# Kernel tuning notes

Measured on AMD Instinct MI355X. Metric: run time of the kernel, lower is better.

The kernel has to match this reference:

```python
import jax, jax.numpy as jnp
import numpy as np

ALPHA = 0.2  # LeakyReLU negative slope
NEG_INF = -1.0e12


def setup_inputs() -> dict:
    key = jax.random.key(0)
    ks = jax.random.split(key, 8)
    N, F, D, H, M, Q = 4096, 512, 64, 4, 2, 128
    x = jax.random.normal(ks[0], (N, F), dtype=jnp.float32)
    adj = jax.random.randint(ks[1], (M, N, N), 0, 2, dtype=jnp.int32)
    W = jax.random.normal(ks[2], (H, F, D), dtype=jnp.float32) * 0.07
    a1 = jax.random.normal(ks[3], (H, D), dtype=jnp.float32) * 0.15
    a2 = jax.random.normal(ks[4], (H, D), dtype=jnp.float32) * 0.15
    Ws = jax.random.normal(ks[5], (H * D, Q), dtype=jnp.float32) * 0.1
    bs = jax.random.normal(ks[6], (1, Q), dtype=jnp.float32) * 0.1
    q_sem = jax.random.normal(ks[7], (Q, 1), dtype=jnp.float32) * 0.15
    return {"x": x, "adj": adj, "W": W, "a1": a1, "a2": a2,
            "Ws": Ws, "bs": bs, "q_sem": q_sem}


def reference(x, adj, W, a1, a2, Ws, bs, q_sem):
    N = x.shape[0]
    # Wh is identical across meta-paths (dropout disabled / eval mode)
    Wh = jnp.einsum('nf,hfd->hnd', x, W)            # [H,N,D]
    s1 = jnp.einsum('hnd,hd->hn', Wh, a1)           # Wh @ a[:D]
    s2 = jnp.einsum('hnd,hd->hn', Wh, a2)           # Wh @ a[D:]

    def metapath(adj_m):
        # e[h,i,j] = leaky_relu(s1[h,i] + s2[h,j]); mask by adjacency
        e = jax.nn.leaky_relu(s1[:, :, None] + s2[:, None, :], negative_slope=ALPHA)
        e = jnp.where(adj_m[None, :, :] > 0, e, NEG_INF)
        att = jax.nn.softmax(e, axis=2)             # softmax over neighbors (dim=1 in torch [N,N])
        h = jax.nn.elu(jnp.einsum('hnm,hmd->hnd', att, Wh))
        return jnp.transpose(h, (1, 0, 2)).reshape(N, -1)  # concat heads -> [N, H*D]

    Z = jax.vmap(metapath)(adj)                     # [M, N, H*D]
    z = jnp.transpose(Z, (1, 0, 2))                 # [N, M, H*D]

    # Semantic attention (faithful to original, incl. softmax over dim=1 of [M,1])
    Whs = jnp.tanh(jnp.einsum('nmf,fq->nmq', z, Ws) + bs)   # [N,M,Q]
    w = jnp.einsum('nmq,qo->nmo', Whs, q_sem).mean(0)        # [M,1]
    beta = jax.nn.softmax(w, axis=1)                          # [M,1]
    return (beta[None, :, :] * z).sum(axis=1)                 # [N, H*D]
```

## Files before the change

kernel.cpp:

```cpp
#include <hip/hip_runtime.h>
#include <hip/hip_fp16.h>
#include <stdint.h>

#define NN 4096
#define FF 512
#define DD 64
#define HH 4
#define MM 2
#define LOG2E 1.44269504088896340736f
#define ALPHA_LR 0.2f

typedef float f32x4 __attribute__((ext_vector_type(4)));
typedef _Float16 f16x8 __attribute__((ext_vector_type(8)));
typedef _Float16 f16x2 __attribute__((ext_vector_type(2)));

union H4 { ushort4 u; _Float16 h[4]; };
union V8 { f16x8 v; f16x2 p[4]; };

__device__ inline float fast_exp2(float x) { return __builtin_amdgcn_exp2f(x); }
__device__ inline float fast_rcp(float x) { return __builtin_amdgcn_rcpf(x); }
__device__ inline f32x4 mfma16(f16x8 a, f16x8 b, f32x4 c) {
    return __builtin_amdgcn_mfma_f32_16x16x32_f16(a, b, c, 0, 0, 0);
}
__device__ inline f16x2 pkrtz(float a, float b) {
    return __builtin_bit_cast(f16x2, __builtin_amdgcn_cvt_pkrtz(a, b));
}
__device__ inline uint32_t enc_f32(float f) {
    uint32_t u = __float_as_uint(f);
    return (u & 0x80000000u) ? ~u : (u | 0x80000000u);
}
__device__ inline float dec_f32(uint32_t k) {
    uint32_t u = (k & 0x80000000u) ? (k ^ 0x80000000u) : ~k;
    return __uint_as_float(u);
}

__global__ __launch_bounds__(256) void k_conv_x(const float* __restrict__ x,
                                                _Float16* __restrict__ xh,
                                                uint32_t* __restrict__ m4a) {
    int t = blockIdx.x * 256 + threadIdx.x;
    if (t < HH) m4a[t] = 0u;
    float4 v = ((const float4*)x)[t];
    H4 o;
    o.h[0] = (_Float16)v.x; o.h[1] = (_Float16)v.y;
    o.h[2] = (_Float16)v.z; o.h[3] = (_Float16)v.w;
    ((ushort4*)xh)[t] = o.u;
}

__global__ __launch_bounds__(256) void k_conv_w(const float* __restrict__ W,
                                                _Float16* __restrict__ wt) {
    int t = blockIdx.x * 256 + threadIdx.x;
    int c = t >> 9, f = t & 511;
    int h = c >> 6, d = c & 63;
    wt[t] = (_Float16)W[(h * FF + f) * DD + d];
}

__global__ __launch_bounds__(256) void k_pack(const int* __restrict__ adj,
                                              unsigned long long* __restrict__ bitsT) {
    const long long total = (long long)MM * NN * NN;
    const long long stride = 2048LL * 256;
    long long tid = (long long)blockIdx.x * 256 + threadIdx.x;
    for (long long e = tid; e < total; e += stride) {
        unsigned long long msk = __ballot(adj[e] != 0);
        if ((threadIdx.x & 63) == 0) {
            long long q = e >> 6;
            int m  = (int)(q >> 18);
            int rem = (int)(q & 262143);
            int i  = rem >> 6;
            int jw = rem & 63;
            bitsT[((size_t)m * 64 + jw) * NN + i] = msk;
        }
    }
}

__global__ __launch_bounds__(512) void k_wh(const _Float16* __restrict__ xh,
                                            const _Float16* __restrict__ wt,
                                            _Float16* __restrict__ whT) {
    const int wave = threadIdx.x >> 6;
    const int h    = wave & 3;
    const int th   = wave >> 2;
    const int lane = threadIdx.x & 63;
    const int iL   = lane & 15;
    const int quad = lane >> 4;
    const int i0   = blockIdx.x * 16;

    f32x4 acc[2];
    acc[0] = (f32x4){0.f, 0.f, 0.f, 0.f};
    acc[1] = (f32x4){0.f, 0.f, 0.f, 0.f};

    const _Float16* arow  = xh + (size_t)(i0 + iL) * FF + quad * 8;
    const _Float16* bbase = wt + (size_t)(h * 64 + th * 32 + iL) * FF + quad * 8;

    for (int kc = 0; kc < FF; kc += 32) {
        f16x8 a = *(const f16x8*)(arow + kc);
        #pragma unroll
        for (int u = 0; u < 2; ++u) {
            f16x8 b = *(const f16x8*)(bbase + (size_t)(16 * u) * FF + kc);
            acc[u] = mfma16(a, b, acc[u]);
        }
    }
    #pragma unroll
    for (int u = 0; u < 2; ++u) {
        H4 o;
        #pragma unroll
        for (int r = 0; r < 4; ++r) o.h[r] = (_Float16)acc[u][r];
        *(ushort4*)(whT + (size_t)(h * 64 + th * 32 + 16 * u + iL) * NN + i0 + quad * 4) = o.u;
    }
}

__global__ __launch_bounds__(64) void k_s(const _Float16* __restrict__ whT,
                                          const float* __restrict__ a1,
                                          const float* __restrict__ a2,
                                          float* __restrict__ s1L,
                                          float* __restrict__ s2L,
                                          uint32_t* __restrict__ m4a) {
    int b = blockIdx.x;
    int h = b >> 6;
    int n = (b & 63) * 64 + threadIdx.x;
    float s1 = 0.f, s2 = 0.f;
    #pragma unroll 8
    for (int d = 0; d < DD; ++d) {
        float w = (float)whT[(size_t)(h * 64 + d) * NN + n];
        s1 += w * a1[h * 64 + d];
        s2 += w * a2[h * 64 + d];
    }
    float s2l = s2 * LOG2E;
    s1L[h * NN + n] = s1 * LOG2E;
    s2L[h * NN + n] = s2l;
    float mx = s2l;
    #pragma unroll
    for (int off = 32; off > 0; off >>= 1) mx = fmaxf(mx, __shfl_down(mx, off));
    if (threadIdx.x == 0) atomicMax(m4a + h, enc_f32(mx));
}

__global__ __launch_bounds__(512, 2) void k_attn(const _Float16* __restrict__ whT,
                                                 const float* __restrict__ s1L,
                                                 const float* __restrict__ s2L,
                                                 const uint32_t* __restrict__ m4a,
                                                 const unsigned long long* __restrict__ bitsT,
                                                 float* __restrict__ out) {
    __shared__ __align__(16) float xr[4][MM][4][16][16];
    __shared__ __align__(16) float dr[4][MM][16];

    const int tid  = threadIdx.x;
    const int wave = tid >> 6;
    const int lane = tid & 63;
    const int iL   = lane & 15;
    const int quad = lane >> 4;
    const int h    = blockIdx.x & 3;
    const int i0   = (blockIdx.x >> 2) * 64;

    const float m4 = dec_f32(m4a[h]);
    float A[4], B[4];
    #pragma unroll
    for (int s = 0; s < 4; ++s) {
        float s1i = s1L[h * NN + i0 + 16 * s + iL];
        float vv  = s1i + m4;
        float cii = fmaxf(vv, ALPHA_LR * vv);
        A[s] = s1i - cii;
        B[s] = ALPHA_LR * s1i - cii;
    }

    f32x4 acc[4][MM][4];
    f32x4 accD[4][MM];
    #pragma unroll
    for (int s = 0; s < 4; ++s)
        #pragma unroll
        for (int m = 0; m < MM; ++m) {
            accD[s][m] = (f32x4){0.f, 0.f, 0.f, 0.f};
            #pragma unroll
            for (int t = 0; t < 4; ++t) acc[s][m][t] = (f32x4){0.f, 0.f, 0.f, 0.f};
        }

    f16x8 bones;
    #pragma unroll
    for (int e = 0; e < 8; ++e) bones[e] = (_Float16)1.0f;

    const float* s2row = s2L + h * NN;
    const _Float16* brow = whT + (size_t)(h * 64 + iL) * NN;
    const int qshift = quad * 8;
    const int jbase = wave * 512;

    const unsigned long long* pB[MM][4];
    #pragma unroll
    for (int m = 0; m < MM; ++m)
        #pragma unroll
        for (int s = 0; s < 4; ++s)
            pB[m][s] = bitsT + (size_t)m * 64 * NN + i0 + 16 * s + iL;

    for (int it = 0; it < 8; ++it) {
        const int jc = jbase + it * 64;
        const int jw = jc >> 6;
        unsigned long long bm[MM][4];
        #pragma unroll
        for (int m = 0; m < MM; ++m)
            #pragma unroll
            for (int s = 0; s < 4; ++s)
                bm[m][s] = pB[m][s][(size_t)jw * NN];

        #pragma unroll
        for (int half = 0; half < 2; ++half) {
            const int jb = jc + 32 * half;
            f16x8 bfr[4];
            #pragma unroll
            for (int t = 0; t < 4; ++t)
                bfr[t] = *(const f16x8*)(brow + (size_t)(16 * t) * NN + jb + qshift);

            const float* s2p = s2row + jb + qshift;
            float4 sa = *(const float4*)s2p;
            float4 sb = *(const float4*)(s2p + 4);
            float s2v[8] = {sa.x, sa.y, sa.z, sa.w, sb.x, sb.y, sb.z, sb.w};
            const int shft = 32 * half + qshift;

            #pragma unroll
            for (int s = 0; s < 4; ++s) {
                float p[8];
                #pragma unroll
                for (int e = 0; e < 8; ++e) {
                    float arg = fmaxf(s2v[e] + A[s], __builtin_fmaf(ALPHA_LR, s2v[e], B[s]));
                    p[e] = fast_exp2(arg);
                }
                uint32_t rs0 = (uint32_t)(bm[0][s] >> shft);
                uint32_t rs1 = (uint32_t)(bm[1][s] >> shft);
                V8 a0, a1v;
                #pragma unroll
                for (int e = 0; e < 4; ++e) {
                    float q0 = (rs0 & (1u << (2 * e)))     ? p[2 * e]     : 0.f;
                    float q1 = (rs0 & (1u << (2 * e + 1))) ? p[2 * e + 1] : 0.f;
                    float r0 = (rs1 & (1u << (2 * e)))     ? p[2 * e]     : 0.f;
                    float r1 = (rs1 & (1u << (2 * e + 1))) ? p[2 * e + 1] : 0.f;
                    a0.p[e]  = pkrtz(q0, q1);
                    a1v.p[e] = pkrtz(r0, r1);
                }
                #pragma unroll
                for (int t = 0; t < 4; ++t) {
                    acc[s][0][t] = mfma16(a0.v, bfr[t], acc[s][0][t]);
                    acc[s][1][t] = mfma16(a1v.v, bfr[t], acc[s][1][t]);
                }
                accD[s][0] = mfma16(a0.v, bones, accD[s][0]);
                accD[s][1] = mfma16(a1v.v, bones, accD[s][1]);
            }
        }
    }

    #define STORE_SLOT(sl, s)                                                 \
        { _Pragma("unroll") for (int m = 0; m < MM; ++m) {                    \
              _Pragma("unroll") for (int t = 0; t < 4; ++t)                   \
                  *(f32x4*)&xr[sl][m][t][iL][quad * 4] = acc[s][m][t];        \
              if (iL == 0) *(f32x4*)&dr[sl][m][quad * 4] = accD[s][m]; } }
    #define ADD_SLOT(sl, s)                                                   \
        { _Pragma("unroll") for (int m = 0; m < MM; ++m) {                    \
              _Pragma("unroll") for (int t = 0; t < 4; ++t)                   \
                  acc[s][m][t] += *(const f32x4*)&xr[sl][m][t][iL][quad * 4]; \
              accD[s][m] += *(const f32x4*)&dr[sl][m][quad * 4]; } }

    for (int s = 0; s < 4; ++s) {
        __syncthreads();
        if (wave >= 4) STORE_SLOT(wave - 4, s);
        __syncthreads();
        if (wave < 4) ADD_SLOT(wave, s);
        __syncthreads();
        if (wave >= 2 && wave < 4) STORE_SLOT(wave - 2, s);
        __syncthreads();
        if (wave < 2) ADD_SLOT(wave, s);
        __syncthreads();
        if (wave == 1) STORE_SLOT(0, s);
        __syncthreads();
        if (wave == 0) {
            ADD_SLOT(0, s);
            const int i0s = i0 + 16 * s;
            #pragma unroll
            for (int t = 0; t < 4; ++t) {
                #pragma unroll
                for (int r = 0; r < 4; ++r) {
                    float v0 = acc[s][0][t][r] * fast_rcp(accD[s][0][r]);
                    float v1 = acc[s][1][t][r] * fast_rcp(accD[s][1][r]);
                    float e0 = v0 > 0.f ? v0 : (fast_exp2(v0 * LOG2E) - 1.f);
                    float e1 = v1 > 0.f ? v1 : (fast_exp2(v1 * LOG2E) - 1.f);
                    out[(size_t)(i0s + quad * 4 + r) * (HH * DD) + h * 64 + 16 * t + iL] = e0 + e1;
                }
            }
        }
    }
    #undef STORE_SLOT
    #undef ADD_SLOT
}

extern "C" void kernel_launch(void* const* d_in, const int* in_sizes, int n_in,
                              void* d_out, int out_size, void* d_ws, size_t ws_size,
                              hipStream_t stream) {
    const float* x   = (const float*)d_in[0];
    const int*   adj = (const int*)d_in[1];
    const float* W   = (const float*)d_in[2];
    const float* a1  = (const float*)d_in[3];
    const float* a2  = (const float*)d_in[4];
    float* out = (float*)d_out;

    char* ws = (char*)d_ws;
    _Float16* xh   = (_Float16*)(ws);
    _Float16* wt   = (_Float16*)(ws + 4194304);
    _Float16* whT  = (_Float16*)(ws + 4456448);
    float*    s1L  = (float*)(ws + 6553600);
    float*    s2L  = (float*)(ws + 6619136);
    uint32_t* m4a  = (uint32_t*)(ws + 6684672);
    unsigned long long* bitsT = (unsigned long long*)(ws + 6750208);

    hipLaunchKernelGGL(k_conv_x, dim3(2048), dim3(256), 0, stream, x, xh, m4a);
    hipLaunchKernelGGL(k_conv_w, dim3(512), dim3(256), 0, stream, W, wt);
    hipLaunchKernelGGL(k_pack, dim3(2048), dim3(256), 0, stream, adj, bitsT);
    hipLaunchKernelGGL(k_wh, dim3(256), dim3(512), 0, stream, xh, wt, whT);
    hipLaunchKernelGGL(k_s, dim3(256), dim3(64), 0, stream, whT, a1, a2, s1L, s2L, m4a);
    hipLaunchKernelGGL(k_attn, dim3(256), dim3(512), 0, stream, whT, s1L, s2L, m4a, bitsT, out);
}
```

Baseline: 287.9 us.

## Fuse prep kernels, fold score projection into Wh GEMM, use fp16 attention math

Merges the three conversion and packing kernels into one launch and folds the s1/s2 score computation, including the per-head max, into the Wh GEMM epilogue, so two launches and a re-read of whT go away. The attention inner loop now computes the LeakyReLU argument and exp2 in packed fp16 and masks with bitwise ANDs instead of fp32 math plus selects and converts, which cuts VALU work in the hot loop. s2 is stored as fp16, which halves its loads. The cost is lower precision in the attention logits and exponentials, with possible accuracy drift.

```diff
diff --git a/kernel.cpp b/kernel.cpp
--- a/kernel.cpp
+++ b/kernel.cpp
@@ -14,17 +14,16 @@
 typedef _Float16 f16x8 __attribute__((ext_vector_type(8)));
 typedef _Float16 f16x2 __attribute__((ext_vector_type(2)));
 
+extern "C" __device__ _Float16 __ocml_exp2_f16(_Float16);
+
 union H4 { ushort4 u; _Float16 h[4]; };
-union V8 { f16x8 v; f16x2 p[4]; };
+union W8 { f16x8 v; uint32_t w[4]; f16x2 p[4]; };
 
 __device__ inline float fast_exp2(float x) { return __builtin_amdgcn_exp2f(x); }
 __device__ inline float fast_rcp(float x) { return __builtin_amdgcn_rcpf(x); }
 __device__ inline f32x4 mfma16(f16x8 a, f16x8 b, f32x4 c) {
     return __builtin_amdgcn_mfma_f32_16x16x32_f16(a, b, c, 0, 0, 0);
 }
-__device__ inline f16x2 pkrtz(float a, float b) {
-    return __builtin_bit_cast(f16x2, __builtin_amdgcn_cvt_pkrtz(a, b));
-}
 __device__ inline uint32_t enc_f32(float f) {
     uint32_t u = __float_as_uint(f);
     return (u & 0x80000000u) ? ~u : (u | 0x80000000u);
@@ -33,48 +32,59 @@
     uint32_t u = (k & 0x80000000u) ? (k ^ 0x80000000u) : ~k;
     return __uint_as_float(u);
 }
-
-__global__ __launch_bounds__(256) void k_conv_x(const float* __restrict__ x,
-                                                _Float16* __restrict__ xh,
-                                                uint32_t* __restrict__ m4a) {
-    int t = blockIdx.x * 256 + threadIdx.x;
-    if (t < HH) m4a[t] = 0u;
-    float4 v = ((const float4*)x)[t];
-    H4 o;
-    o.h[0] = (_Float16)v.x; o.h[1] = (_Float16)v.y;
-    o.h[2] = (_Float16)v.z; o.h[3] = (_Float16)v.w;
-    ((ushort4*)xh)[t] = o.u;
-}
-
-__global__ __launch_bounds__(256) void k_conv_w(const float* __restrict__ W,
-                                                _Float16* __restrict__ wt) {
-    int t = blockIdx.x * 256 + threadIdx.x;
-    int c = t >> 9, f = t & 511;
-    int h = c >> 6, d = c & 63;
-    wt[t] = (_Float16)W[(h * FF + f) * DD + d];
-}
-
-__global__ __launch_bounds__(256) void k_pack(const int* __restrict__ adj,
-                                              unsigned long long* __restrict__ bitsT) {
-    const long long total = (long long)MM * NN * NN;
-    const long long stride = 2048LL * 256;
-    long long tid = (long long)blockIdx.x * 256 + threadIdx.x;
-    for (long long e = tid; e < total; e += stride) {
-        unsigned long long msk = __ballot(adj[e] != 0);
-        if ((threadIdx.x & 63) == 0) {
-            long long q = e >> 6;
-            int m  = (int)(q >> 18);
-            int rem = (int)(q & 262143);
-            int i  = rem >> 6;
-            int jw = rem & 63;
-            bitsT[((size_t)m * 64 + jw) * NN + i] = msk;
-        }
+__device__ inline uint32_t mpair(uint32_t rs, int k) {
+    return (((rs >> (2 * k)) & 1u) ? 0x0000FFFFu : 0u) |
+           (((rs >> (2 * k + 1)) & 1u) ? 0xFFFF0000u : 0u);
+}
+
+__global__ __launch_bounds__(256) void k_prep(const float* __restrict__ x,
+                                              const int* __restrict__ adj,
+                                              const float* __restrict__ W,
+                                              _Float16* __restrict__ xh,
+                                              _Float16* __restrict__ wt,
+                                              unsigned long long* __restrict__ bitsT,
+                                              uint32_t* __restrict__ m4a) {
+    const int bid = blockIdx.x;
+    if (bid < 2048) {
+        const long long total = (long long)MM * NN * NN;
+        const long long stride = 2048LL * 256;
+        long long tid = (long long)bid * 256 + threadIdx.x;
+        for (long long e = tid; e < total; e += stride) {
+            unsigned long long msk = __ballot(adj[e] != 0);
+            if ((threadIdx.x & 63) == 0) {
+                long long q = e >> 6;
+                int m  = (int)(q >> 18);
+                int rem = (int)(q & 262143);
+                int i  = rem >> 6;
+                int jw = rem & 63;
+                bitsT[((size_t)m * 64 + jw) * NN + i] = msk;
+            }
+        }
+    } else if (bid < 4096) {
+        int t = (bid - 2048) * 256 + threadIdx.x;
+        if (t < HH) m4a[t] = 0u;
+        float4 v = ((const float4*)x)[t];
+        H4 o;
+        o.h[0] = (_Float16)v.x; o.h[1] = (_Float16)v.y;
+        o.h[2] = (_Float16)v.z; o.h[3] = (_Float16)v.w;
+        ((ushort4*)xh)[t] = o.u;
+    } else {
+        int t = (bid - 4096) * 256 + threadIdx.x;
+        int c = t >> 9, f = t & 511;
+        int h = c >> 6, d = c & 63;
+        wt[t] = (_Float16)W[(h * FF + f) * DD + d];
     }
 }
 
 __global__ __launch_bounds__(512) void k_wh(const _Float16* __restrict__ xh,
                                             const _Float16* __restrict__ wt,
-                                            _Float16* __restrict__ whT) {
+                                            const float* __restrict__ a1,
+                                            const float* __restrict__ a2,
+                                            _Float16* __restrict__ whT,
+                                            float* __restrict__ s1L,
+                                            _Float16* __restrict__ s2h,
+                                            uint32_t* __restrict__ m4a) {
+    __shared__ float sred[8][2][16];
     const int wave = threadIdx.x >> 6;
     const int h    = wave & 3;
     const int th   = wave >> 2;
@@ -105,36 +115,44 @@
         for (int r = 0; r < 4; ++r) o.h[r] = (_Float16)acc[u][r];
         *(ushort4*)(whT + (size_t)(h * 64 + th * 32 + 16 * u + iL) * NN + i0 + quad * 4) = o.u;
     }
-}
-
-__global__ __launch_bounds__(64) void k_s(const _Float16* __restrict__ whT,
-                                          const float* __restrict__ a1,
-                                          const float* __restrict__ a2,
-                                          float* __restrict__ s1L,
-                                          float* __restrict__ s2L,
-                                          uint32_t* __restrict__ m4a) {
-    int b = blockIdx.x;
-    int h = b >> 6;
-    int n = (b & 63) * 64 + threadIdx.x;
-    float s1 = 0.f, s2 = 0.f;
-    #pragma unroll 8
-    for (int d = 0; d < DD; ++d) {
-        float w = (float)whT[(size_t)(h * 64 + d) * NN + n];
-        s1 += w * a1[h * 64 + d];
-        s2 += w * a2[h * 64 + d];
-    }
-    float s2l = s2 * LOG2E;
-    s1L[h * NN + n] = s1 * LOG2E;
-    s2L[h * NN + n] = s2l;
-    float mx = s2l;
-    #pragma unroll
-    for (int off = 32; off > 0; off >>= 1) mx = fmaxf(mx, __shfl_down(mx, off));
-    if (threadIdx.x == 0) atomicMax(m4a + h, enc_f32(mx));
+
+    const float a1v0 = a1[h * 64 + th * 32 + iL];
+    const float a1v1 = a1[h * 64 + th * 32 + 16 + iL];
+    const float a2v0 = a2[h * 64 + th * 32 + iL];
+    const float a2v1 = a2[h * 64 + th * 32 + 16 + iL];
+    #pragma unroll
+    for (int r = 0; r < 4; ++r) {
+        float p1 = acc[0][r] * a1v0 + acc[1][r] * a1v1;
+        float p2 = acc[0][r] * a2v0 + acc[1][r] * a2v1;
+        #pragma unroll
+        for (int off = 1; off < 16; off <<= 1) {
+            p1 += __shfl_xor(p1, off);
+            p2 += __shfl_xor(p2, off);
+        }
+        if (iL == 0) {
+            sred[wave][0][quad * 4 + r] = p1;
+            sred[wave][1][quad * 4 + r] = p2;
+        }
+    }
+    __syncthreads();
+    if (threadIdx.x < 64) {
+        int h2  = threadIdx.x >> 4;
+        int idx = threadIdx.x & 15;
+        float s1 = sred[h2][0][idx] + sred[h2 + 4][0][idx];
+        float s2 = sred[h2][1][idx] + sred[h2 + 4][1][idx];
+        float s2l = s2 * LOG2E;
+        s1L[h2 * NN + i0 + idx] = s1 * LOG2E;
+        s2h[h2 * NN + i0 + idx] = (_Float16)s2l;
+        float mx = s2l;
+        #pragma unroll
+        for (int off = 1; off < 16; off <<= 1) mx = fmaxf(mx, __shfl_xor(mx, off));
+        if (idx == 0) atomicMax(m4a + h2, enc_f32(mx));
+    }
 }
 
 __global__ __launch_bounds__(512, 2) void k_attn(const _Float16* __restrict__ whT,
                                                  const float* __restrict__ s1L,
-                                                 const float* __restrict__ s2L,
+                                                 const _Float16* __restrict__ s2h,
                                                  const uint32_t* __restrict__ m4a,
                                                  const unsigned long long* __restrict__ bitsT,
                                                  float* __restrict__ out) {
@@ -150,15 +168,18 @@
     const int i0   = (blockIdx.x >> 2) * 64;
 
     const float m4 = dec_f32(m4a[h]);
-    float A[4], B[4];
+    f16x2 A2[4], B2[4];
     #pragma unroll
     for (int s = 0; s < 4; ++s) {
         float s1i = s1L[h * NN + i0 + 16 * s + iL];
         float vv  = s1i + m4;
         float cii = fmaxf(vv, ALPHA_LR * vv);
-        A[s] = s1i - cii;
-        B[s] = ALPHA_LR * s1i - cii;
-    }
+        _Float16 a = (_Float16)(s1i - cii);
+        _Float16 b = (_Float16)(ALPHA_LR * s1i - cii);
+        A2[s] = (f16x2){a, a};
+        B2[s] = (f16x2){b, b};
+    }
+    const f16x2 al2 = (f16x2){(_Float16)ALPHA_LR, (_Float16)ALPHA_LR};
 
     f32x4 acc[4][MM][4];
     f32x4 accD[4][MM];
@@ -175,7 +196,7 @@
     #pragma unroll
     for (int e = 0; e < 8; ++e) bones[e] = (_Float16)1.0f;
 
-    const float* s2row = s2L + h * NN;
+    const _Float16* s2row = s2h + h * NN;
     const _Float16* brow = whT + (size_t)(h * 64 + iL) * NN;
     const int qshift = quad * 8;
     const int jbase = wave * 512;
@@ -205,31 +226,24 @@
             for (int t = 0; t < 4; ++t)
                 bfr[t] = *(const f16x8*)(brow + (size_t)(16 * t) * NN + jb + qshift);
 
-            const float* s2p = s2row + jb + qshift;
-            float4 sa = *(const float4*)s2p;
-            float4 sb = *(const float4*)(s2p + 4);
-            float s2v[8] = {sa.x, sa.y, sa.z, sa.w, sb.x, sb.y, sb.z, sb.w};
+            const W8 s2v = *(const W8*)(s2row + jb + qshift);
             const int shft = 32 * half + qshift;
 
             #pragma unroll
             for (int s = 0; s < 4; ++s) {
-                float p[8];
-                #pragma unroll
-                for (int e = 0; e < 8; ++e) {
-                    float arg = fmaxf(s2v[e] + A[s], __builtin_fmaf(ALPHA_LR, s2v[e], B[s]));
-                    p[e] = fast_exp2(arg);
-                }
                 uint32_t rs0 = (uint32_t)(bm[0][s] >> shft);
                 uint32_t rs1 = (uint32_t)(bm[1][s] >> shft);
-                V8 a0, a1v;
+                W8 a0, a1v;
                 #pragma unroll
-                for (int e = 0; e < 4; ++e) {
-                    float q0 = (rs0 & (1u << (2 * e)))     ? p[2 * e]     : 0.f;
-                    float q1 = (rs0 & (1u << (2 * e + 1))) ? p[2 * e + 1] : 0.f;
-                    float r0 = (rs1 & (1u << (2 * e)))     ? p[2 * e]     : 0.f;
-                    float r1 = (rs1 & (1u << (2 * e + 1))) ? p[2 * e + 1] : 0.f;
-                    a0.p[e]  = pkrtz(q0, q1);
-                    a1v.p[e] = pkrtz(r0, r1);
+                for (int k = 0; k < 4; ++k) {
+                    f16x2 z = s2v.p[k] + A2[s];
+                    f16x2 l = al2 * s2v.p[k] + B2[s];
+                    _Float16 m0 = z[0] > l[0] ? z[0] : l[0];
+                    _Float16 m1 = z[1] > l[1] ? z[1] : l[1];
+                    f16x2 p = (f16x2){__ocml_exp2_f16(m0), __ocml_exp2_f16(m1)};
+                    uint32_t pw = __builtin_bit_cast(uint32_t, p);
+                    a0.w[k]  = pw & mpair(rs0, k);
+                    a1v.w[k] = pw & mpair(rs1, k);
                 }
                 #pragma unroll
                 for (int t = 0; t < 4; ++t) {
@@ -300,14 +314,14 @@
     _Float16* wt   = (_Float16*)(ws + 4194304);
     _Float16* whT  = (_Float16*)(ws + 4456448);
     float*    s1L  = (float*)(ws + 6553600);
-    float*    s2L  = (float*)(ws + 6619136);
+    _Float16* s2h  = (_Float16*)(ws + 6619136);
     uint32_t* m4a  = (uint32_t*)(ws + 6684672);
     unsigned long long* bitsT = (unsigned long long*)(ws + 6750208);
 
-    hipLaunchKernelGGL(k_conv_x, dim3(2048), dim3(256), 0, stream, x, xh, m4a);
-    hipLaunchKernelGGL(k_conv_w, dim3(512), dim3(256), 0, stream, W, wt);
-    hipLaunchKernelGGL(k_pack, dim3(2048), dim3(256), 0, stream, adj, bitsT);
-    hipLaunchKernelGGL(k_wh, dim3(256), dim3(512), 0, stream, xh, wt, whT);
-    hipLaunchKernelGGL(k_s, dim3(256), dim3(64), 0, stream, whT, a1, a2, s1L, s2L, m4a);
-    hipLaunchKernelGGL(k_attn, dim3(256), dim3(512), 0, stream, whT, s1L, s2L, m4a, bitsT, out);
-}
+    hipLaunchKernelGGL(k_prep, dim3(4608), dim3(256), 0, stream,
+                       x, adj, W, xh, wt, bitsT, m4a);
+    hipLaunchKernelGGL(k_wh, dim3(256), dim3(512), 0, stream,
+                       xh, wt, a1, a2, whT, s1L, s2h, m4a);
+    hipLaunchKernelGGL(k_attn, dim3(256), dim3(512), 0, stream,
+                       whT, s1L, s2h, m4a, bitsT, out);
+}
```

Result: faster. 276.1 us (-4.1%).
